# Optimization experiments

Hardware: AMD Instinct MI355X
Metric: run time of the kernel (lower is better)

The kernel has to match this reference:

```python
import jax, jax.numpy as jnp
import numpy as np

N = 100000
NNZ = 3200000
NFEAT, NHID, NCLASS = 512, 256, 41

def setup_inputs() -> dict:
    key = jax.random.key(0)
    ks = jax.random.split(key, 8)
    x = jax.random.normal(ks[0], (N, NFEAT), dtype=jnp.float32)
    adj_rows = jnp.sort(jax.random.randint(ks[1], (NNZ,), 0, N))
    adj_cols = jax.random.randint(ks[2], (NNZ,), 0, N)
    adj_vals = jax.random.uniform(ks[3], (NNZ,), dtype=jnp.float32) / 32.0  # ~normalized adj
    s1 = 1.0 / np.sqrt(NHID)
    s2 = 1.0 / np.sqrt(NCLASS)
    w1 = jax.random.uniform(ks[4], (NFEAT, NHID), minval=-s1, maxval=s1, dtype=jnp.float32)
    b1 = jax.random.uniform(ks[5], (NHID,), minval=-s1, maxval=s1, dtype=jnp.float32)
    w2 = jax.random.uniform(ks[6], (NHID, NCLASS), minval=-s2, maxval=s2, dtype=jnp.float32)
    b2 = jax.random.uniform(ks[7], (NCLASS,), minval=-s2, maxval=s2, dtype=jnp.float32)
    return {"x": x, "adj_rows": adj_rows, "adj_cols": adj_cols, "adj_vals": adj_vals,
            "w1": w1, "b1": b1, "w2": w2, "b2": b2}

def spmm(rows, cols, vals, dense):
    # sparse [N,N] @ dense [N,D] via gather + segment_sum
    gathered = dense[cols] * vals[:, None]  # [nnz, D]
    return jax.ops.segment_sum(gathered, rows, num_segments=N)

def reference(x, adj_rows, adj_cols, adj_vals, w1, b1, w2, b2):
    # layer 1: A(XW) + b, relu  (GraphConvolution)
    h = spmm(adj_rows, adj_cols, adj_vals, x @ w1) + b1
    h = jax.nn.relu(h)
    # dropout: inference mode (training=False) -> identity
    # layer 2: (AX)W + b  (GraphConvolution2)
    out = spmm(adj_rows, adj_cols, adj_vals, h) @ w2 + b2
    return jax.nn.log_softmax(out, axis=1)
```

## Files before the change

kernel.cpp:

```cpp
#include <hip/hip_runtime.h>
#include <math.h>

#define N_NODES 100000
#define NNZ_E   3200000
#define NFEAT   512
#define NHID    256
#define NCLASS  41
#define NC_PAD  48
#define P_STRIDE 64

typedef __attribute__((ext_vector_type(8))) short   short8;
typedef __attribute__((ext_vector_type(4))) float   f32x4;
typedef __attribute__((ext_vector_type(2))) float   f32x2;

typedef __attribute__((address_space(1))) const unsigned int gu32;
typedef __attribute__((address_space(3))) unsigned int lu32;

__device__ __forceinline__ unsigned short f2bf(float f) {
    unsigned u = __builtin_bit_cast(unsigned, f);
    unsigned r = u + 0x7fffu + ((u >> 16) & 1u);
    return (unsigned short)(r >> 16);
}
__device__ __forceinline__ unsigned char f2fp8(float f) {
    return (unsigned char)(__builtin_amdgcn_cvt_pk_fp8_f32(f, 0.f, 0, false) & 0xff);
}
__device__ __forceinline__ unsigned pk4(float a, float b, float c, float d) {
    unsigned u = __builtin_amdgcn_cvt_pk_fp8_f32(a, b, 0, false);
    return (unsigned)__builtin_amdgcn_cvt_pk_fp8_f32(c, d, (int)u, true);
}

__global__ __launch_bounds__(256) void prep_misc_kernel(const int* __restrict__ rows,
                                                        const float* __restrict__ w1,
                                                        const float* __restrict__ w2,
                                                        int* __restrict__ row_ptr,
                                                        unsigned char* __restrict__ w1q,
                                                        unsigned short* __restrict__ w2t) {
    int b = blockIdx.x;
    if (b < 392) {
        int r = b * 256 + threadIdx.x;
        if (r > N_NODES) return;
        int lo = 0, hi = NNZ_E;
        while (lo < hi) {
            int mid = (lo + hi) >> 1;
            if (rows[mid] < r) lo = mid + 1; else hi = mid;
        }
        row_ptr[r] = lo;
        return;
    }
    b -= 392;
    if (b < 512) {
        int tid = b * 256 + threadIdx.x;
        int n = tid >> 9, k = tid & 511;
        w1q[tid] = f2fp8(w1[k * NHID + n]);
        return;
    }
    b -= 512;
    {
        int t2 = b * 256 + threadIdx.x;
        int n = t2 >> 8, k = t2 & 255;
        w2t[t2] = (n < NCLASS) ? f2bf(w2[k * NCLASS + n]) : (unsigned short)0;
    }
}

__global__ __launch_bounds__(512) void gemm1_kernel(const float* __restrict__ x,
                                                    const unsigned char* __restrict__ w1q,
                                                    unsigned char* __restrict__ xw) {
    __shared__ unsigned char As[8192];
    __shared__ unsigned char Bs[16384];

    const int tid  = threadIdx.x;
    const int wv   = tid >> 6;
    const int lane = tid & 63;
    const int l15  = lane & 15;
    const int quad = lane >> 4;
    const int wvM  = wv >> 2;
    const int wvN  = wv & 3;
    const int rb   = blockIdx.x * 128;

    const int ar = tid >> 2;
    const int aq = tid & 3;
    int arow = rb + ar; if (arow >= N_NODES) arow = N_NODES - 1;
    const float* asrc = x + (long)arow * NFEAT + aq * 16;
    unsigned char* adst0 = As + ar * 64 + (((2 * aq + 0) ^ (ar & 6)) * 8);
    unsigned char* adst1 = As + ar * 64 + (((2 * aq + 1) ^ (ar & 6)) * 8);

    const int bn0 = (wv * 2 + 0) * 16 + (lane >> 2);
    const int bn1 = (wv * 2 + 1) * 16 + (lane >> 2);
    const int bg0 = (lane & 3) ^ ((bn0 >> 1) & 3);
    const int bg1 = (lane & 3) ^ ((bn1 >> 1) & 3);
    const unsigned char* bsrc0 = w1q + (long)bn0 * NFEAT + bg0 * 16;
    const unsigned char* bsrc1 = w1q + (long)bn1 * NFEAT + bg1 * 16;

    f32x4 acc[4][4] = {};

    float4 fr0 = *(const float4*)(asrc);
    float4 fr1 = *(const float4*)(asrc + 4);
    float4 fr2 = *(const float4*)(asrc + 8);
    float4 fr3 = *(const float4*)(asrc + 12);

    for (int c = 0; c < 8; c++) {
        const int kc = c * 64;
        __builtin_amdgcn_global_load_lds((gu32*)(bsrc0 + kc), (lu32*)(Bs + (wv * 2 + 0) * 1024), 16, 0, 0);
        __builtin_amdgcn_global_load_lds((gu32*)(bsrc1 + kc), (lu32*)(Bs + (wv * 2 + 1) * 1024), 16, 0, 0);
        unsigned u0 = pk4(fr0.x, fr0.y, fr0.z, fr0.w);
        unsigned u1 = pk4(fr1.x, fr1.y, fr1.z, fr1.w);
        unsigned u2 = pk4(fr2.x, fr2.y, fr2.z, fr2.w);
        unsigned u3 = pk4(fr3.x, fr3.y, fr3.z, fr3.w);
        *(unsigned long long*)adst0 = (unsigned long long)u0 | ((unsigned long long)u1 << 32);
        *(unsigned long long*)adst1 = (unsigned long long)u2 | ((unsigned long long)u3 << 32);
        if (c < 7) {
            fr0 = *(const float4*)(asrc + kc + 64);
            fr1 = *(const float4*)(asrc + kc + 68);
            fr2 = *(const float4*)(asrc + kc + 72);
            fr3 = *(const float4*)(asrc + kc + 76);
        }
        __syncthreads();

        unsigned long long a[4][2], b[4][2];
#pragma unroll
        for (int mt = 0; mt < 4; mt++) {
            int row = wvM * 64 + mt * 16 + l15;
#pragma unroll
            for (int ks = 0; ks < 2; ks++) {
                int p8 = (ks * 4 + quad) ^ (row & 6);
                a[mt][ks] = *(const unsigned long long*)(As + row * 64 + p8 * 8);
            }
        }
#pragma unroll
        for (int nt = 0; nt < 4; nt++) {
            int nr = wvN * 64 + nt * 16 + l15;
#pragma unroll
            for (int ks = 0; ks < 2; ks++) {
                int p8 = (ks * 4 + quad) ^ (nr & 6);
                b[nt][ks] = *(const unsigned long long*)(Bs + nr * 64 + p8 * 8);
            }
        }
#pragma unroll
        for (int ks = 0; ks < 2; ks++)
#pragma unroll
            for (int nt = 0; nt < 4; nt++)
#pragma unroll
                for (int mt = 0; mt < 4; mt++)
                    acc[mt][nt] = __builtin_amdgcn_mfma_f32_16x16x32_fp8_fp8(
                        (long)a[mt][ks], (long)b[nt][ks], acc[mt][nt], 0, 0, 0);
        __syncthreads();
    }

#pragma unroll
    for (int mt = 0; mt < 4; mt++) {
        int row0 = rb + wvM * 64 + mt * 16 + quad * 4;
#pragma unroll
        for (int nt = 0; nt < 4; nt++) {
            int col = wvN * 64 + nt * 16 + l15;
#pragma unroll
            for (int r = 0; r < 4; r++) {
                int row = row0 + r;
                if (row < N_NODES)
                    xw[(long)row * NHID + col] = f2fp8(acc[mt][nt][r]);
            }
        }
    }
}

__global__ __launch_bounds__(256) void spmm1_kernel(const unsigned char* __restrict__ xw,
                                                    const int* __restrict__ row_ptr,
                                                    const int* __restrict__ cols,
                                                    const float* __restrict__ vals,
                                                    const float* __restrict__ b1,
                                                    unsigned short* __restrict__ h) {
    int row = blockIdx.x * 4 + (threadIdx.x >> 6);
    if (row >= N_NODES) return;
    int lane = threadIdx.x & 63;
    int e0 = row_ptr[row], e1 = row_ptr[row + 1];

    float a0 = 0.f, a1 = 0.f, a2 = 0.f, a3 = 0.f;
    for (int base = e0; base < e1; base += 64) {
        int   myc = 0;
        float myv = 0.f;
        int idx = base + lane;
        if (idx < e1) { myc = cols[idx]; myv = vals[idx]; }
        int cnt = e1 - base; if (cnt > 64) cnt = 64;
        int j = 0;
        for (; j + 8 <= cnt; j += 8) {
            int c[8]; float v[8];
#pragma unroll
            for (int u = 0; u < 8; u++) { c[u] = __shfl(myc, j + u); v[u] = __shfl(myv, j + u); }
            unsigned q[8];
#pragma unroll
            for (int u = 0; u < 8; u++) q[u] = *(const unsigned*)(xw + (long)c[u] * NHID + lane * 4);
#pragma unroll
            for (int u = 0; u < 8; u++) {
                f32x2 lo = __builtin_amdgcn_cvt_pk_f32_fp8((int)q[u], false);
                f32x2 hi = __builtin_amdgcn_cvt_pk_f32_fp8((int)q[u], true);
                a0 += v[u] * lo[0];
                a1 += v[u] * lo[1];
                a2 += v[u] * hi[0];
                a3 += v[u] * hi[1];
            }
        }
        for (; j < cnt; j++) {
            int   c = __shfl(myc, j);
            float v = __shfl(myv, j);
            unsigned q = *(const unsigned*)(xw + (long)c * NHID + lane * 4);
            f32x2 lo = __builtin_amdgcn_cvt_pk_f32_fp8((int)q, false);
            f32x2 hi = __builtin_amdgcn_cvt_pk_f32_fp8((int)q, true);
            a0 += v * lo[0];
            a1 += v * lo[1];
            a2 += v * hi[0];
            a3 += v * hi[1];
        }
    }
    float4 bv = *(const float4*)(b1 + lane * 4);
    a0 = fmaxf(a0 + bv.x, 0.f);
    a1 = fmaxf(a1 + bv.y, 0.f);
    a2 = fmaxf(a2 + bv.z, 0.f);
    a3 = fmaxf(a3 + bv.w, 0.f);
    uint2 o;
    o.x = (unsigned)f2bf(a0) | ((unsigned)f2bf(a1) << 16);
    o.y = (unsigned)f2bf(a2) | ((unsigned)f2bf(a3) << 16);
    *(uint2*)(h + (long)row * NHID + lane * 4) = o;
}

__global__ __launch_bounds__(256) void gemm2_kernel(const unsigned short* __restrict__ h,
                                                    const unsigned short* __restrict__ w2t,
                                                    unsigned char* __restrict__ p) {
    int rt = blockIdx.x * 4 + (threadIdx.x >> 6);
    int row0 = rt * 16;
    if (row0 >= N_NODES) return;
    int lane = threadIdx.x & 63;
    int l15 = lane & 15, quad = lane >> 4;

    int arow = row0 + l15; if (arow >= N_NODES) arow = N_NODES - 1;
    f32x4 acc[3] = {};
#pragma unroll
    for (int kc = 0; kc < NHID; kc += 32) {
        short8 a = *(const short8*)(h + (long)arow * NHID + kc + quad * 8);
#pragma unroll
        for (int nt = 0; nt < 3; nt++) {
            short8 b = *(const short8*)(w2t + (long)(nt * 16 + l15) * NHID + kc + quad * 8);
            acc[nt] = __builtin_amdgcn_mfma_f32_16x16x32_bf16(a, b, acc[nt], 0, 0, 0);
        }
    }
#pragma unroll
    for (int nt = 0; nt < 3; nt++) {
        int col = nt * 16 + l15;
#pragma unroll
        for (int r = 0; r < 4; r++) {
            int row = row0 + quad * 4 + r;
            if (row < N_NODES)
                p[(long)row * P_STRIDE + col] = f2fp8(acc[nt][r]);
        }
    }
}

__global__ __launch_bounds__(256) void spmm2_kernel(const unsigned char* __restrict__ p,
                                                    const int* __restrict__ row_ptr,
                                                    const int* __restrict__ cols,
                                                    const float* __restrict__ vals,
                                                    const float* __restrict__ b2,
                                                    float* __restrict__ out) {
    int row = blockIdx.x * 4 + (threadIdx.x >> 6);
    if (row >= N_NODES) return;
    int lane = threadIdx.x & 63;
    int e = lane >> 5;
    int t = lane & 31;
    int e0 = row_ptr[row], e1 = row_ptr[row + 1];

    float a0 = 0.f, a1 = 0.f, a2 = 0.f, a3 = 0.f;
    for (int base = e0; base < e1; base += 64) {
        int   myc = 0;
        float myv = 0.f;
        int idx = base + lane;
        if (idx < e1) {
            myc = __builtin_nontemporal_load(cols + idx);
            myv = __builtin_nontemporal_load(vals + idx);
        }
        int cnt = e1 - base; if (cnt > 64) cnt = 64;
        int j = 0;
        for (; j + 8 <= cnt; j += 8) {
            int c[4]; float v[4];
#pragma unroll
            for (int u = 0; u < 4; u++) {
                c[u] = __shfl(myc, j + 2 * u + e);
                v[u] = __shfl(myv, j + 2 * u + e);
            }
            unsigned q[4];
#pragma unroll
            for (int u = 0; u < 4; u++)
                q[u] = (t < 12) ? *(const unsigned*)(p + (long)c[u] * P_STRIDE + 4 * t) : 0u;
#pragma unroll
            for (int u = 0; u < 4; u++) {
                f32x2 lo = __builtin_amdgcn_cvt_pk_f32_fp8((int)q[u], false);
                f32x2 hi = __builtin_amdgcn_cvt_pk_f32_fp8((int)q[u], true);
                a0 += v[u] * lo[0];
                a1 += v[u] * lo[1];
                a2 += v[u] * hi[0];
                a3 += v[u] * hi[1];
            }
        }
        for (; j < cnt; j += 2) {
            int jj = j + e;
            int jc = jj < cnt ? jj : cnt - 1;
            int   c = __shfl(myc, jc);
            float v = __shfl(myv, jc);
            if (jj >= cnt) v = 0.f;
            unsigned q = (t < 12) ? *(const unsigned*)(p + (long)c * P_STRIDE + 4 * t) : 0u;
            f32x2 lo = __builtin_amdgcn_cvt_pk_f32_fp8((int)q, false);
            f32x2 hi = __builtin_amdgcn_cvt_pk_f32_fp8((int)q, true);
            a0 += v * lo[0];
            a1 += v * lo[1];
            a2 += v * hi[0];
            a3 += v * hi[1];
        }
    }
    a0 += __shfl_xor(a0, 32);
    a1 += __shfl_xor(a1, 32);
    a2 += __shfl_xor(a2, 32);
    a3 += __shfl_xor(a3, 32);

    int c0 = 4 * t, c1 = 4 * t + 1, c2 = 4 * t + 2, c3 = 4 * t + 3;
    float l0 = (c0 < NCLASS) ? a0 + b2[c0] : -__builtin_inff();
    float l1 = (c1 < NCLASS) ? a1 + b2[c1] : -__builtin_inff();
    float l2 = (c2 < NCLASS) ? a2 + b2[c2] : -__builtin_inff();
    float l3 = (c3 < NCLASS) ? a3 + b2[c3] : -__builtin_inff();
    float m = fmaxf(fmaxf(l0, l1), fmaxf(l2, l3));
#pragma unroll
    for (int s = 16; s; s >>= 1) m = fmaxf(m, __shfl_xor(m, s));
    float esum = ((c0 < NCLASS) ? __expf(l0 - m) : 0.f)
               + ((c1 < NCLASS) ? __expf(l1 - m) : 0.f)
               + ((c2 < NCLASS) ? __expf(l2 - m) : 0.f)
               + ((c3 < NCLASS) ? __expf(l3 - m) : 0.f);
#pragma unroll
    for (int s = 16; s; s >>= 1) esum += __shfl_xor(esum, s);
    float lse = m + __logf(esum);
    if (e == 0) {
        long ob = (long)row * NCLASS;
        if (c0 < NCLASS) out[ob + c0] = l0 - lse;
        if (c1 < NCLASS) out[ob + c1] = l1 - lse;
        if (c2 < NCLASS) out[ob + c2] = l2 - lse;
        if (c3 < NCLASS) out[ob + c3] = l3 - lse;
    }
}

extern "C" void kernel_launch(void* const* d_in, const int* in_sizes, int n_in,
                              void* d_out, int out_size, void* d_ws, size_t ws_size,
                              hipStream_t stream) {
    const float* x        = (const float*)d_in[0];
    const int*   adj_rows = (const int*)  d_in[1];
    const int*   adj_cols = (const int*)  d_in[2];
    const float* adj_vals = (const float*)d_in[3];
    const float* w1       = (const float*)d_in[4];
    const float* b1       = (const float*)d_in[5];
    const float* w2       = (const float*)d_in[6];
    const float* b2       = (const float*)d_in[7];
    float* out = (float*)d_out;

    char* ws = (char*)d_ws;
    unsigned char*  w1q     = (unsigned char*) (ws);
    unsigned short* w2t     = (unsigned short*)(ws + 0x20000);
    int*            row_ptr = (int*)           (ws + 0x26000);
    unsigned short* hbuf    = (unsigned short*)(ws + 0x90000);
    unsigned char*  xw      = (unsigned char*) (ws + 0x3180000);
    unsigned char*  p       = (unsigned char*) (ws + 0x3180000);

    prep_misc_kernel<<<392 + 512 + 48, 256, 0, stream>>>(adj_rows, w1, w2, row_ptr, w1q, w2t);
    gemm1_kernel<<<(N_NODES + 127) / 128, 512, 0, stream>>>(x, w1q, xw);
    spmm1_kernel<<<(N_NODES + 3) / 4, 256, 0, stream>>>(xw, row_ptr, adj_cols, adj_vals, b1, hbuf);
    gemm2_kernel<<<((N_NODES + 15) / 16 + 3) / 4, 256, 0, stream>>>(hbuf, w2t, p);
    spmm2_kernel<<<(N_NODES + 3) / 4, 256, 0, stream>>>(p, row_ptr, adj_cols, adj_vals, b2, out);
}
```

Before: 552.9 us.

## Double-buffer gemm1 LDS tiles and repack spmm2 lanes for four-edge parallel gathers

gemm1 now uses two LDS buffers for A and B, so the global loads and fp8 conversion for the next K chunk overlap the MFMA compute on the current one. This needs only one barrier per iteration. spmm2 is reorganized so each 16-lane group handles one edge, giving four edges per wave step instead of two. Edge indices and values are loaded directly with a software-prefetched register pipeline rather than through shuffles. The cost is double the LDS use in gemm1, which may lower occupancy, plus 4 of every 16 lanes idle in spmm2's gathers.

Measured after the change: 559.0 us. About the same (+1.1%).

```diff
diff --git a/kernel.cpp b/kernel.cpp
--- a/kernel.cpp
+++ b/kernel.cpp
@@ -65,8 +65,8 @@
 __global__ __launch_bounds__(512) void gemm1_kernel(const float* __restrict__ x,
                                                     const unsigned char* __restrict__ w1q,
                                                     unsigned char* __restrict__ xw) {
-    __shared__ unsigned char As[8192];
-    __shared__ unsigned char Bs[16384];
+    __shared__ unsigned char As[2][8192];
+    __shared__ unsigned char Bs[2][16384];
 
     const int tid  = threadIdx.x;
     const int wv   = tid >> 6;
@@ -81,8 +81,8 @@
     const int aq = tid & 3;
     int arow = rb + ar; if (arow >= N_NODES) arow = N_NODES - 1;
     const float* asrc = x + (long)arow * NFEAT + aq * 16;
-    unsigned char* adst0 = As + ar * 64 + (((2 * aq + 0) ^ (ar & 6)) * 8);
-    unsigned char* adst1 = As + ar * 64 + (((2 * aq + 1) ^ (ar & 6)) * 8);
+    const int aoff0 = ar * 64 + (((2 * aq + 0) ^ (ar & 6)) * 8);
+    const int aoff1 = ar * 64 + (((2 * aq + 1) ^ (ar & 6)) * 8);
 
     const int bn0 = (wv * 2 + 0) * 16 + (lane >> 2);
     const int bn1 = (wv * 2 + 1) * 16 + (lane >> 2);
@@ -90,61 +90,74 @@
     const int bg1 = (lane & 3) ^ ((bn1 >> 1) & 3);
     const unsigned char* bsrc0 = w1q + (long)bn0 * NFEAT + bg0 * 16;
     const unsigned char* bsrc1 = w1q + (long)bn1 * NFEAT + bg1 * 16;
+    const int boff0 = (wv * 2 + 0) * 1024;
+    const int boff1 = (wv * 2 + 1) * 1024;
 
     f32x4 acc[4][4] = {};
-
-    float4 fr0 = *(const float4*)(asrc);
-    float4 fr1 = *(const float4*)(asrc + 4);
-    float4 fr2 = *(const float4*)(asrc + 8);
-    float4 fr3 = *(const float4*)(asrc + 12);
-
-    for (int c = 0; c < 8; c++) {
-        const int kc = c * 64;
-        __builtin_amdgcn_global_load_lds((gu32*)(bsrc0 + kc), (lu32*)(Bs + (wv * 2 + 0) * 1024), 16, 0, 0);
-        __builtin_amdgcn_global_load_lds((gu32*)(bsrc1 + kc), (lu32*)(Bs + (wv * 2 + 1) * 1024), 16, 0, 0);
-        unsigned u0 = pk4(fr0.x, fr0.y, fr0.z, fr0.w);
-        unsigned u1 = pk4(fr1.x, fr1.y, fr1.z, fr1.w);
-        unsigned u2 = pk4(fr2.x, fr2.y, fr2.z, fr2.w);
-        unsigned u3 = pk4(fr3.x, fr3.y, fr3.z, fr3.w);
-        *(unsigned long long*)adst0 = (unsigned long long)u0 | ((unsigned long long)u1 << 32);
-        *(unsigned long long*)adst1 = (unsigned long long)u2 | ((unsigned long long)u3 << 32);
+    float4 fr0, fr1, fr2, fr3;
+
+#define LOAD_A_REGS(kc)  do { fr0 = *(const float4*)(asrc + (kc)); \
+                              fr1 = *(const float4*)(asrc + (kc) + 4); \
+                              fr2 = *(const float4*)(asrc + (kc) + 8); \
+                              fr3 = *(const float4*)(asrc + (kc) + 12); } while (0)
+#define CVT_A(buf)       do { unsigned u0 = pk4(fr0.x, fr0.y, fr0.z, fr0.w); \
+                              unsigned u1 = pk4(fr1.x, fr1.y, fr1.z, fr1.w); \
+                              unsigned u2 = pk4(fr2.x, fr2.y, fr2.z, fr2.w); \
+                              unsigned u3 = pk4(fr3.x, fr3.y, fr3.z, fr3.w); \
+                              *(unsigned long long*)(&As[buf][aoff0]) = (unsigned long long)u0 | ((unsigned long long)u1 << 32); \
+                              *(unsigned long long*)(&As[buf][aoff1]) = (unsigned long long)u2 | ((unsigned long long)u3 << 32); } while (0)
+#define ISSUE_B(kc, buf) do { __builtin_amdgcn_global_load_lds((gu32*)(bsrc0 + (kc)), (lu32*)(&Bs[buf][boff0]), 16, 0, 0); \
+                              __builtin_amdgcn_global_load_lds((gu32*)(bsrc1 + (kc)), (lu32*)(&Bs[buf][boff1]), 16, 0, 0); } while (0)
+#define COMPUTE(buf)     do { unsigned long long a[4][2], b[4][2]; \
+                              _Pragma("unroll") \
+                              for (int mt = 0; mt < 4; mt++) { \
+                                  int row = wvM * 64 + mt * 16 + l15; \
+                                  _Pragma("unroll") \
+                                  for (int ks = 0; ks < 2; ks++) { \
+                                      int p8 = (ks * 4 + quad) ^ (row & 6); \
+                                      a[mt][ks] = *(const unsigned long long*)(&As[buf][row * 64 + p8 * 8]); \
+                                  } \
+                              } \
+                              _Pragma("unroll") \
+                              for (int nt = 0; nt < 4; nt++) { \
+                                  int nr = wvN * 64 + nt * 16 + l15; \
+                                  _Pragma("unroll") \
+                                  for (int ks = 0; ks < 2; ks++) { \
+                                      int p8 = (ks * 4 + quad) ^ (nr & 6); \
+                                      b[nt][ks] = *(const unsigned long long*)(&Bs[buf][nr * 64 + p8 * 8]); \
+                                  } \
+                              } \
+                              _Pragma("unroll") \
+                              for (int ks = 0; ks < 2; ks++) \
+                                  _Pragma("unroll") \
+                                  for (int nt = 0; nt < 4; nt++) \
+                                      _Pragma("unroll") \
+                                      for (int mt = 0; mt < 4; mt++) \
+                                          acc[mt][nt] = __builtin_amdgcn_mfma_f32_16x16x32_fp8_fp8( \
+                                              (long)a[mt][ks], (long)b[nt][ks], acc[mt][nt], 0, 0, 0); } while (0)
+
+    LOAD_A_REGS(0);
+    ISSUE_B(0, 0);
+    CVT_A(0);
+    __syncthreads();
+    LOAD_A_REGS(64);
+    ISSUE_B(64, 1);
+    COMPUTE(0);
+
+    for (int c = 1; c < 8; c++) {
+        const int cur = c & 1;
+        CVT_A(cur);
+        __syncthreads();
         if (c < 7) {
-            fr0 = *(const float4*)(asrc + kc + 64);
-            fr1 = *(const float4*)(asrc + kc + 68);
-            fr2 = *(const float4*)(asrc + kc + 72);
-            fr3 = *(const float4*)(asrc + kc + 76);
-        }
-        __syncthreads();
-
-        unsigned long long a[4][2], b[4][2];
-#pragma unroll
-        for (int mt = 0; mt < 4; mt++) {
-            int row = wvM * 64 + mt * 16 + l15;
-#pragma unroll
-            for (int ks = 0; ks < 2; ks++) {
-                int p8 = (ks * 4 + quad) ^ (row & 6);
-                a[mt][ks] = *(const unsigned long long*)(As + row * 64 + p8 * 8);
-            }
-        }
-#pragma unroll
-        for (int nt = 0; nt < 4; nt++) {
-            int nr = wvN * 64 + nt * 16 + l15;
-#pragma unroll
-            for (int ks = 0; ks < 2; ks++) {
-                int p8 = (ks * 4 + quad) ^ (nr & 6);
-                b[nt][ks] = *(const unsigned long long*)(Bs + nr * 64 + p8 * 8);
-            }
-        }
-#pragma unroll
-        for (int ks = 0; ks < 2; ks++)
-#pragma unroll
-            for (int nt = 0; nt < 4; nt++)
-#pragma unroll
-                for (int mt = 0; mt < 4; mt++)
-                    acc[mt][nt] = __builtin_amdgcn_mfma_f32_16x16x32_fp8_fp8(
-                        (long)a[mt][ks], (long)b[nt][ks], acc[mt][nt], 0, 0, 0);
-        __syncthreads();
-    }
+            LOAD_A_REGS((c + 1) * 64);
+            ISSUE_B((c + 1) * 64, cur ^ 1);
+        }
+        COMPUTE(cur);
+    }
+#undef LOAD_A_REGS
+#undef CVT_A
+#undef ISSUE_B
+#undef COMPUTE
 
 #pragma unroll
     for (int mt = 0; mt < 4; mt++) {
@@ -262,61 +275,45 @@
     int row = blockIdx.x * 4 + (threadIdx.x >> 6);
     if (row >= N_NODES) return;
     int lane = threadIdx.x & 63;
-    int e = lane >> 5;
-    int t = lane & 31;
-    int e0 = row_ptr[row], e1 = row_ptr[row + 1];
+    int e = lane >> 4;
+    int t = lane & 15;
+    int e0 = __builtin_amdgcn_readfirstlane(row_ptr[row]);
+    int e1 = __builtin_amdgcn_readfirstlane(row_ptr[row + 1]);
+    const unsigned toff = (unsigned)(t << 2);
 
     float a0 = 0.f, a1 = 0.f, a2 = 0.f, a3 = 0.f;
-    for (int base = e0; base < e1; base += 64) {
-        int   myc = 0;
-        float myv = 0.f;
-        int idx = base + lane;
-        if (idx < e1) {
-            myc = __builtin_nontemporal_load(cols + idx);
-            myv = __builtin_nontemporal_load(vals + idx);
-        }
-        int cnt = e1 - base; if (cnt > 64) cnt = 64;
-        int j = 0;
-        for (; j + 8 <= cnt; j += 8) {
-            int c[4]; float v[4];
-#pragma unroll
-            for (int u = 0; u < 4; u++) {
-                c[u] = __shfl(myc, j + 2 * u + e);
-                v[u] = __shfl(myv, j + 2 * u + e);
-            }
-            unsigned q[4];
-#pragma unroll
-            for (int u = 0; u < 4; u++)
-                q[u] = (t < 12) ? *(const unsigned*)(p + (long)c[u] * P_STRIDE + 4 * t) : 0u;
-#pragma unroll
-            for (int u = 0; u < 4; u++) {
-                f32x2 lo = __builtin_amdgcn_cvt_pk_f32_fp8((int)q[u], false);
-                f32x2 hi = __builtin_amdgcn_cvt_pk_f32_fp8((int)q[u], true);
-                a0 += v[u] * lo[0];
-                a1 += v[u] * lo[1];
-                a2 += v[u] * hi[0];
-                a3 += v[u] * hi[1];
-            }
-        }
-        for (; j < cnt; j += 2) {
-            int jj = j + e;
-            int jc = jj < cnt ? jj : cnt - 1;
-            int   c = __shfl(myc, jc);
-            float v = __shfl(myv, jc);
-            if (jj >= cnt) v = 0.f;
-            unsigned q = (t < 12) ? *(const unsigned*)(p + (long)c * P_STRIDE + 4 * t) : 0u;
-            f32x2 lo = __builtin_amdgcn_cvt_pk_f32_fp8((int)q, false);
-            f32x2 hi = __builtin_amdgcn_cvt_pk_f32_fp8((int)q, true);
-            a0 += v * lo[0];
-            a1 += v * lo[1];
-            a2 += v * hi[0];
-            a3 += v * hi[1];
-        }
-    }
-    a0 += __shfl_xor(a0, 32);
-    a1 += __shfl_xor(a1, 32);
-    a2 += __shfl_xor(a2, 32);
-    a3 += __shfl_xor(a3, 32);
+    if (e0 < e1) {
+        const int em1 = e1 - 1;
+        int i0 = e0 + e;     int i0c = i0 < e1 ? i0 : em1;
+        int i1 = e0 + 4 + e; int i1c = i1 < e1 ? i1 : em1;
+        int   ca = __builtin_nontemporal_load(cols + i0c);
+        float va = __builtin_nontemporal_load(vals + i0c);
+        int   cb = __builtin_nontemporal_load(cols + i1c);
+        float vb = __builtin_nontemporal_load(vals + i1c);
+        for (int j = e0; j < e1; j += 8) {
+            int n0 = j + 8 + e;  int n0c = n0 < e1 ? n0 : em1;
+            int n1 = j + 12 + e; int n1c = n1 < e1 ? n1 : em1;
+            int   cc = __builtin_nontemporal_load(cols + n0c);
+            float vc = __builtin_nontemporal_load(vals + n0c);
+            int   cd = __builtin_nontemporal_load(cols + n1c);
+            float vd = __builtin_nontemporal_load(vals + n1c);
+            unsigned q0 = (t < 12) ? *(const unsigned*)(p + (long)ca * P_STRIDE + toff) : 0u;
+            unsigned q1 = (t < 12) ? *(const unsigned*)(p + (long)cb * P_STRIDE + toff) : 0u;
+            float v0 = (j + e     < e1) ? va : 0.f;
+            float v1 = (j + 4 + e < e1) ? vb : 0.f;
+            f32x2 lo0 = __builtin_amdgcn_cvt_pk_f32_fp8((int)q0, false);
+            f32x2 hi0 = __builtin_amdgcn_cvt_pk_f32_fp8((int)q0, true);
+            f32x2 lo1 = __builtin_amdgcn_cvt_pk_f32_fp8((int)q1, false);
+            f32x2 hi1 = __builtin_amdgcn_cvt_pk_f32_fp8((int)q1, true);
+            a0 += v0 * lo0[0]; a1 += v0 * lo0[1]; a2 += v0 * hi0[0]; a3 += v0 * hi0[1];
+            a0 += v1 * lo1[0]; a1 += v1 * lo1[1]; a2 += v1 * hi1[0]; a3 += v1 * hi1[1];
+            ca = cc; va = vc; cb = cd; vb = vd;
+        }
+    }
+    a0 += __shfl_xor(a0, 16); a1 += __shfl_xor(a1, 16);
+    a2 += __shfl_xor(a2, 16); a3 += __shfl_xor(a3, 16);
+    a0 += __shfl_xor(a0, 32); a1 += __shfl_xor(a1, 32);
+    a2 += __shfl_xor(a2, 32); a3 += __shfl_xor(a3, 32);
 
     int c0 = 4 * t, c1 = 4 * t + 1, c2 = 4 * t + 2, c3 = 4 * t + 3;
     float l0 = (c0 < NCLASS) ? a0 + b2[c0] : -__builtin_inff();
@@ -325,13 +322,13 @@
     float l3 = (c3 < NCLASS) ? a3 + b2[c3] : -__builtin_inff();
     float m = fmaxf(fmaxf(l0, l1), fmaxf(l2, l3));
 #pragma unroll
-    for (int s = 16; s; s >>= 1) m = fmaxf(m, __shfl_xor(m, s));
+    for (int s = 8; s; s >>= 1) m = fmaxf(m, __shfl_xor(m, s));
     float esum = ((c0 < NCLASS) ? __expf(l0 - m) : 0.f)
                + ((c1 < NCLASS) ? __expf(l1 - m) : 0.f)
                + ((c2 < NCLASS) ? __expf(l2 - m) : 0.f)
                + ((c3 < NCLASS) ? __expf(l3 - m) : 0.f);
 #pragma unroll
-    for (int s = 16; s; s >>= 1) esum += __shfl_xor(esum, s);
+    for (int s = 8; s; s >>= 1) esum += __shfl_xor(esum, s);
     float lse = m + __logf(esum);
     if (e == 0) {
         long ob = (long)row * NCLASS;
```

## Fuse SpMM1 with the second GEMM via LDS and restructure SpMM2 edge loop

Applied to the files above, without the earlier changes.

Merges spmm1 and gemm2 into one kernel. Each block aggregates 32 rows into bf16 in shared memory, then two waves run the MFMA projection to the 48-class padded output, so the 51 MB h buffer never goes to global memory. SpMM2 now splits each wave into 4 groups of 16 lanes that handle 4 edges at a time, and prefetches cols and vals one iteration ahead in place of loading them in 64-wide chunks and shuffling them. The fused kernel has 8 serial rows per wave and only half its waves do the GEMM, so per-block latency and occupancy change.

Result: no change. 555.8 us (+0.5%).

```diff
diff --git a/kernel.cpp b/kernel.cpp
--- a/kernel.cpp
+++ b/kernel.cpp
@@ -162,93 +162,93 @@
     }
 }
 
-__global__ __launch_bounds__(256) void spmm1_kernel(const unsigned char* __restrict__ xw,
-                                                    const int* __restrict__ row_ptr,
-                                                    const int* __restrict__ cols,
-                                                    const float* __restrict__ vals,
-                                                    const float* __restrict__ b1,
-                                                    unsigned short* __restrict__ h) {
-    int row = blockIdx.x * 4 + (threadIdx.x >> 6);
-    if (row >= N_NODES) return;
-    int lane = threadIdx.x & 63;
-    int e0 = row_ptr[row], e1 = row_ptr[row + 1];
-
-    float a0 = 0.f, a1 = 0.f, a2 = 0.f, a3 = 0.f;
-    for (int base = e0; base < e1; base += 64) {
-        int   myc = 0;
-        float myv = 0.f;
-        int idx = base + lane;
-        if (idx < e1) { myc = cols[idx]; myv = vals[idx]; }
-        int cnt = e1 - base; if (cnt > 64) cnt = 64;
-        int j = 0;
-        for (; j + 8 <= cnt; j += 8) {
-            int c[8]; float v[8];
-#pragma unroll
-            for (int u = 0; u < 8; u++) { c[u] = __shfl(myc, j + u); v[u] = __shfl(myv, j + u); }
-            unsigned q[8];
-#pragma unroll
-            for (int u = 0; u < 8; u++) q[u] = *(const unsigned*)(xw + (long)c[u] * NHID + lane * 4);
-#pragma unroll
-            for (int u = 0; u < 8; u++) {
-                f32x2 lo = __builtin_amdgcn_cvt_pk_f32_fp8((int)q[u], false);
-                f32x2 hi = __builtin_amdgcn_cvt_pk_f32_fp8((int)q[u], true);
-                a0 += v[u] * lo[0];
-                a1 += v[u] * lo[1];
-                a2 += v[u] * hi[0];
-                a3 += v[u] * hi[1];
-            }
-        }
-        for (; j < cnt; j++) {
-            int   c = __shfl(myc, j);
-            float v = __shfl(myv, j);
-            unsigned q = *(const unsigned*)(xw + (long)c * NHID + lane * 4);
-            f32x2 lo = __builtin_amdgcn_cvt_pk_f32_fp8((int)q, false);
-            f32x2 hi = __builtin_amdgcn_cvt_pk_f32_fp8((int)q, true);
-            a0 += v * lo[0];
-            a1 += v * lo[1];
-            a2 += v * hi[0];
-            a3 += v * hi[1];
-        }
-    }
-    float4 bv = *(const float4*)(b1 + lane * 4);
-    a0 = fmaxf(a0 + bv.x, 0.f);
-    a1 = fmaxf(a1 + bv.y, 0.f);
-    a2 = fmaxf(a2 + bv.z, 0.f);
-    a3 = fmaxf(a3 + bv.w, 0.f);
-    uint2 o;
-    o.x = (unsigned)f2bf(a0) | ((unsigned)f2bf(a1) << 16);
-    o.y = (unsigned)f2bf(a2) | ((unsigned)f2bf(a3) << 16);
-    *(uint2*)(h + (long)row * NHID + lane * 4) = o;
-}
-
-__global__ __launch_bounds__(256) void gemm2_kernel(const unsigned short* __restrict__ h,
-                                                    const unsigned short* __restrict__ w2t,
-                                                    unsigned char* __restrict__ p) {
-    int rt = blockIdx.x * 4 + (threadIdx.x >> 6);
-    int row0 = rt * 16;
-    if (row0 >= N_NODES) return;
-    int lane = threadIdx.x & 63;
-    int l15 = lane & 15, quad = lane >> 4;
-
-    int arow = row0 + l15; if (arow >= N_NODES) arow = N_NODES - 1;
-    f32x4 acc[3] = {};
-#pragma unroll
-    for (int kc = 0; kc < NHID; kc += 32) {
-        short8 a = *(const short8*)(h + (long)arow * NHID + kc + quad * 8);
+__global__ __launch_bounds__(256) void spmm1g_kernel(const unsigned char* __restrict__ xw,
+                                                     const int* __restrict__ row_ptr,
+                                                     const int* __restrict__ cols,
+                                                     const float* __restrict__ vals,
+                                                     const float* __restrict__ b1,
+                                                     const unsigned short* __restrict__ w2t,
+                                                     unsigned char* __restrict__ p) {
+    __shared__ unsigned short hl[32][264];
+
+    const int wv   = threadIdx.x >> 6;
+    const int lane = threadIdx.x & 63;
+    const int row0 = blockIdx.x * 32;
+    const float4 bv = *(const float4*)(b1 + lane * 4);
+
+    for (int r = 0; r < 8; r++) {
+        const int lrow = wv * 8 + r;
+        const int row  = row0 + lrow;
+        int e0 = row_ptr[row], e1 = row_ptr[row + 1];
+
+        float a0 = 0.f, a1 = 0.f, a2 = 0.f, a3 = 0.f;
+        for (int base = e0; base < e1; base += 64) {
+            int   myc = 0;
+            float myv = 0.f;
+            int idx = base + lane;
+            if (idx < e1) { myc = cols[idx]; myv = vals[idx]; }
+            int cnt = e1 - base; if (cnt > 64) cnt = 64;
+            int j = 0;
+            for (; j + 8 <= cnt; j += 8) {
+                int c[8]; float v[8];
+#pragma unroll
+                for (int u = 0; u < 8; u++) { c[u] = __shfl(myc, j + u); v[u] = __shfl(myv, j + u); }
+                unsigned q[8];
+#pragma unroll
+                for (int u = 0; u < 8; u++) q[u] = *(const unsigned*)(xw + (long)c[u] * NHID + lane * 4);
+#pragma unroll
+                for (int u = 0; u < 8; u++) {
+                    f32x2 lo = __builtin_amdgcn_cvt_pk_f32_fp8((int)q[u], false);
+                    f32x2 hi = __builtin_amdgcn_cvt_pk_f32_fp8((int)q[u], true);
+                    a0 += v[u] * lo[0];
+                    a1 += v[u] * lo[1];
+                    a2 += v[u] * hi[0];
+                    a3 += v[u] * hi[1];
+                }
+            }
+            for (; j < cnt; j++) {
+                int   c = __shfl(myc, j);
+                float v = __shfl(myv, j);
+                unsigned q = *(const unsigned*)(xw + (long)c * NHID + lane * 4);
+                f32x2 lo = __builtin_amdgcn_cvt_pk_f32_fp8((int)q, false);
+                f32x2 hi = __builtin_amdgcn_cvt_pk_f32_fp8((int)q, true);
+                a0 += v * lo[0];
+                a1 += v * lo[1];
+                a2 += v * hi[0];
+                a3 += v * hi[1];
+            }
+        }
+        a0 = fmaxf(a0 + bv.x, 0.f);
+        a1 = fmaxf(a1 + bv.y, 0.f);
+        a2 = fmaxf(a2 + bv.z, 0.f);
+        a3 = fmaxf(a3 + bv.w, 0.f);
+        unsigned lo32 = (unsigned)f2bf(a0) | ((unsigned)f2bf(a1) << 16);
+        unsigned hi32 = (unsigned)f2bf(a2) | ((unsigned)f2bf(a3) << 16);
+        unsigned* dst = (unsigned*)&hl[lrow][lane * 4];
+        dst[0] = lo32;
+        dst[1] = hi32;
+    }
+    __syncthreads();
+
+    if (wv < 2) {
+        const int l15 = lane & 15, quad = lane >> 4;
+        f32x4 acc[3] = {};
+#pragma unroll
+        for (int kc = 0; kc < NHID; kc += 32) {
+            short8 a = *(const short8*)(&hl[wv * 16 + l15][kc + quad * 8]);
+#pragma unroll
+            for (int nt = 0; nt < 3; nt++) {
+                short8 b = *(const short8*)(w2t + (long)(nt * 16 + l15) * NHID + kc + quad * 8);
+                acc[nt] = __builtin_amdgcn_mfma_f32_16x16x32_bf16(a, b, acc[nt], 0, 0, 0);
+            }
+        }
+        const int prow0 = row0 + wv * 16 + quad * 4;
 #pragma unroll
         for (int nt = 0; nt < 3; nt++) {
-            short8 b = *(const short8*)(w2t + (long)(nt * 16 + l15) * NHID + kc + quad * 8);
-            acc[nt] = __builtin_amdgcn_mfma_f32_16x16x32_bf16(a, b, acc[nt], 0, 0, 0);
-        }
-    }
-#pragma unroll
-    for (int nt = 0; nt < 3; nt++) {
-        int col = nt * 16 + l15;
-#pragma unroll
-        for (int r = 0; r < 4; r++) {
-            int row = row0 + quad * 4 + r;
-            if (row < N_NODES)
-                p[(long)row * P_STRIDE + col] = f2fp8(acc[nt][r]);
+            int col = nt * 16 + l15;
+#pragma unroll
+            for (int r = 0; r < 4; r++)
+                p[(long)(prow0 + r) * P_STRIDE + col] = f2fp8(acc[nt][r]);
         }
     }
 }
@@ -262,61 +262,45 @@
     int row = blockIdx.x * 4 + (threadIdx.x >> 6);
     if (row >= N_NODES) return;
     int lane = threadIdx.x & 63;
-    int e = lane >> 5;
-    int t = lane & 31;
-    int e0 = row_ptr[row], e1 = row_ptr[row + 1];
+    int e = lane >> 4;
+    int t = lane & 15;
+    int e0 = __builtin_amdgcn_readfirstlane(row_ptr[row]);
+    int e1 = __builtin_amdgcn_readfirstlane(row_ptr[row + 1]);
+    const unsigned toff = (unsigned)(t << 2);
 
     float a0 = 0.f, a1 = 0.f, a2 = 0.f, a3 = 0.f;
-    for (int base = e0; base < e1; base += 64) {
-        int   myc = 0;
-        float myv = 0.f;
-        int idx = base + lane;
-        if (idx < e1) {
-            myc = __builtin_nontemporal_load(cols + idx);
-            myv = __builtin_nontemporal_load(vals + idx);
-        }
-        int cnt = e1 - base; if (cnt > 64) cnt = 64;
-        int j = 0;
-        for (; j + 8 <= cnt; j += 8) {
-            int c[4]; float v[4];
-#pragma unroll
-            for (int u = 0; u < 4; u++) {
-                c[u] = __shfl(myc, j + 2 * u + e);
-                v[u] = __shfl(myv, j + 2 * u + e);
-            }
-            unsigned q[4];
-#pragma unroll
-            for (int u = 0; u < 4; u++)
-                q[u] = (t < 12) ? *(const unsigned*)(p + (long)c[u] * P_STRIDE + 4 * t) : 0u;
-#pragma unroll
-            for (int u = 0; u < 4; u++) {
-                f32x2 lo = __builtin_amdgcn_cvt_pk_f32_fp8((int)q[u], false);
-                f32x2 hi = __builtin_amdgcn_cvt_pk_f32_fp8((int)q[u], true);
-                a0 += v[u] * lo[0];
-                a1 += v[u] * lo[1];
-                a2 += v[u] * hi[0];
-                a3 += v[u] * hi[1];
-            }
-        }
-        for (; j < cnt; j += 2) {
-            int jj = j + e;
-            int jc = jj < cnt ? jj : cnt - 1;
-            int   c = __shfl(myc, jc);
-            float v = __shfl(myv, jc);
-            if (jj >= cnt) v = 0.f;
-            unsigned q = (t < 12) ? *(const unsigned*)(p + (long)c * P_STRIDE + 4 * t) : 0u;
-            f32x2 lo = __builtin_amdgcn_cvt_pk_f32_fp8((int)q, false);
-            f32x2 hi = __builtin_amdgcn_cvt_pk_f32_fp8((int)q, true);
-            a0 += v * lo[0];
-            a1 += v * lo[1];
-            a2 += v * hi[0];
-            a3 += v * hi[1];
-        }
-    }
-    a0 += __shfl_xor(a0, 32);
-    a1 += __shfl_xor(a1, 32);
-    a2 += __shfl_xor(a2, 32);
-    a3 += __shfl_xor(a3, 32);
+    if (e0 < e1) {
+        const int em1 = e1 - 1;
+        int i0 = e0 + e;     int i0c = i0 < e1 ? i0 : em1;
+        int i1 = e0 + 4 + e; int i1c = i1 < e1 ? i1 : em1;
+        int   ca = __builtin_nontemporal_load(cols + i0c);
+        float va = __builtin_nontemporal_load(vals + i0c);
+        int   cb = __builtin_nontemporal_load(cols + i1c);
+        float vb = __builtin_nontemporal_load(vals + i1c);
+        for (int j = e0; j < e1; j += 8) {
+            int n0 = j + 8 + e;  int n0c = n0 < e1 ? n0 : em1;
+            int n1 = j + 12 + e; int n1c = n1 < e1 ? n1 : em1;
+            int   cc = __builtin_nontemporal_load(cols + n0c);
+            float vc = __builtin_nontemporal_load(vals + n0c);
+            int   cd = __builtin_nontemporal_load(cols + n1c);
+            float vd = __builtin_nontemporal_load(vals + n1c);
+            unsigned q0 = (t < 12) ? *(const unsigned*)(p + (long)ca * P_STRIDE + toff) : 0u;
+            unsigned q1 = (t < 12) ? *(const unsigned*)(p + (long)cb * P_STRIDE + toff) : 0u;
+            float v0 = (j + e     < e1) ? va : 0.f;
+            float v1 = (j + 4 + e < e1) ? vb : 0.f;
+            f32x2 lo0 = __builtin_amdgcn_cvt_pk_f32_fp8((int)q0, false);
+            f32x2 hi0 = __builtin_amdgcn_cvt_pk_f32_fp8((int)q0, true);
+            f32x2 lo1 = __builtin_amdgcn_cvt_pk_f32_fp8((int)q1, false);
+            f32x2 hi1 = __builtin_amdgcn_cvt_pk_f32_fp8((int)q1, true);
+            a0 += v0 * lo0[0]; a1 += v0 * lo0[1]; a2 += v0 * hi0[0]; a3 += v0 * hi0[1];
+            a0 += v1 * lo1[0]; a1 += v1 * lo1[1]; a2 += v1 * hi1[0]; a3 += v1 * hi1[1];
+            ca = cc; va = vc; cb = cd; vb = vd;
+        }
+    }
+    a0 += __shfl_xor(a0, 16); a1 += __shfl_xor(a1, 16);
+    a2 += __shfl_xor(a2, 16); a3 += __shfl_xor(a3, 16);
+    a0 += __shfl_xor(a0, 32); a1 += __shfl_xor(a1, 32);
+    a2 += __shfl_xor(a2, 32); a3 += __shfl_xor(a3, 32);
 
     int c0 = 4 * t, c1 = 4 * t + 1, c2 = 4 * t + 2, c3 = 4 * t + 3;
     float l0 = (c0 < NCLASS) ? a0 + b2[c0] : -__builtin_inff();
@@ -325,13 +309,13 @@
     float l3 = (c3 < NCLASS) ? a3 + b2[c3] : -__builtin_inff();
     float m = fmaxf(fmaxf(l0, l1), fmaxf(l2, l3));
 #pragma unroll
-    for (int s = 16; s; s >>= 1) m = fmaxf(m, __shfl_xor(m, s));
+    for (int s = 8; s; s >>= 1) m = fmaxf(m, __shfl_xor(m, s));
     float esum = ((c0 < NCLASS) ? __expf(l0 - m) : 0.f)
                + ((c1 < NCLASS) ? __expf(l1 - m) : 0.f)
                + ((c2 < NCLASS) ? __expf(l2 - m) : 0.f)
                + ((c3 < NCLASS) ? __expf(l3 - m) : 0.f);
 #pragma unroll
-    for (int s = 16; s; s >>= 1) esum += __shfl_xor(esum, s);
+    for (int s = 8; s; s >>= 1) esum += __shfl_xor(esum, s);
     float lse = m + __logf(esum);
     if (e == 0) {
         long ob = (long)row * NCLASS;
@@ -359,13 +343,11 @@
     unsigned char*  w1q     = (unsigned char*) (ws);
     unsigned short* w2t     = (unsigned short*)(ws + 0x20000);
     int*            row_ptr = (int*)           (ws + 0x26000);
-    unsigned short* hbuf    = (unsigned short*)(ws + 0x90000);
+    unsigned char*  p       = (unsigned char*) (ws + 0x90000);
     unsigned char*  xw      = (unsigned char*) (ws + 0x3180000);
-    unsigned char*  p       = (unsigned char*) (ws + 0x3180000);
 
     prep_misc_kernel<<<392 + 512 + 48, 256, 0, stream>>>(adj_rows, w1, w2, row_ptr, w1q, w2t);
     gemm1_kernel<<<(N_NODES + 127) / 128, 512, 0, stream>>>(x, w1q, xw);
-    spmm1_kernel<<<(N_NODES + 3) / 4, 256, 0, stream>>>(xw, row_ptr, adj_cols, adj_vals, b1, hbuf);
-    gemm2_kernel<<<((N_NODES + 15) / 16 + 3) / 4, 256, 0, stream>>>(hbuf, w2t, p);
+    spmm1g_kernel<<<N_NODES / 32, 256, 0, stream>>>(xw, row_ptr, adj_cols, adj_vals, b1, w2t, p);
     spmm2_kernel<<<(N_NODES + 3) / 4, 256, 0, stream>>>(p, row_ptr, adj_cols, adj_vals, b2, out);
 }
```
